# Optimization experiments

Hardware: AMD Instinct MI355X
Metric: run time of the kernel (lower is better)

## Reference

```python
import jax, jax.numpy as jnp
import numpy as np

N, E, B = 30000, 100000, 1024
FXD, FXT, D, H, NOUT = 78, 954, 128, 10, 2


def setup_inputs() -> dict:
    key = jax.random.key(0)
    ks = jax.random.split(key, 24)
    rn = lambda i, shape, s=0.05: jax.random.normal(ks[i], shape, dtype=jnp.float32) * s
    z = lambda shape: jnp.zeros(shape, dtype=jnp.float32)
    batch = ((jnp.arange(N) * B) // N).astype(jnp.int32)  # sorted, every graph id present
    return {
        "x1": rn(0, (N, FXD), 1.0),
        "edge_index1": jax.random.randint(ks[1], (2, E), 0, N, dtype=jnp.int32),
        "batch1": batch,
        "x2": rn(2, (N, FXD), 1.0),
        "edge_index2": jax.random.randint(ks[3], (2, E), 0, N, dtype=jnp.int32),
        "batch2": batch,
        "cell": jax.random.uniform(ks[4], (B, FXT), dtype=jnp.float32),
        "W1": rn(5, (FXD, H * D)), "a_src1": rn(6, (1, H, D)), "a_dst1": rn(7, (1, H, D)), "b1": z((H * D,)),
        # GATConv2: 1280 -> 128, 1 head
        "W2": rn(8, (H * D, D)), "a_src2": rn(9, (1, 1, D)), "a_dst2": rn(10, (1, 1, D)), "b2": z((D,)),
        "Wg": rn(11, (D, D)), "bg": z((D,)),
        "Wr1": rn(12, (FXT, 2048)), "br1": z((2048,)),
        "Wr2": rn(13, (2048, 512)), "br2": z((512,)),
        "Wr3": rn(14, (512, 2 * D)), "br3": z((2 * D,)),
        "Wf1": rn(15, (4 * D, 1024)), "bf1": z((1024,)),
        "Wf2": rn(16, (1024, 512)), "bf2": z((512,)),
        "Wf3": rn(17, (512, 128)), "bf3": z((128,)),
        "Wo": rn(18, (128, NOUT)), "bo": z((NOUT,)),
    }


def gat_conv(x, src, dst, W, a_src, a_dst, bias, heads, ch):
    """PyG GATConv (v1), self-loops already included in src/dst. Concat heads."""
    n = x.shape[0]
    h = (x @ W).reshape(n, heads, ch)                      # [N,H,C]
    alpha_s = jnp.sum(h * a_src, axis=-1)                  # [N,H]
    alpha_d = jnp.sum(h * a_dst, axis=-1)                  # [N,H]
    e = jax.nn.leaky_relu(alpha_s[src] + alpha_d[dst], 0.2)  # [E',H]
    emax = jax.ops.segment_max(e, dst, num_segments=n)     # segment softmax over dst
    ex = jnp.exp(e - emax[dst])
    denom = jax.ops.segment_sum(ex, dst, num_segments=n)
    alpha = ex / (denom[dst] + 1e-16)                      # [E',H]
    msg = h[src] * alpha[:, :, None]                       # [E',H,C]
    out = jax.ops.segment_sum(msg, dst, num_segments=n)    # [N,H,C]
    return out.reshape(n, heads * ch) + bias


def _l2norm(x):
    return x / jnp.maximum(jnp.linalg.norm(x, axis=1, keepdims=True), 1e-12)


def reference(x1, edge_index1, batch1, x2, edge_index2, batch2, cell,
              W1, a_src1, a_dst1, b1, W2, a_src2, a_dst2, b2, Wg, bg,
              Wr1, br1, Wr2, br2, Wr3, br3, Wf1, bf1, Wf2, bf2, Wf3, bf3, Wo, bo):
    def branch(x, ei, batch):
        n = x.shape[0]
        loops = jnp.arange(n, dtype=ei.dtype)              # add_self_loops=True
        src = jnp.concatenate([ei[0], loops])
        dst = jnp.concatenate([ei[1], loops])
        h = jax.nn.elu(gat_conv(x, src, dst, W1, a_src1, a_dst1, b1, H, D))
        h = jax.nn.elu(gat_conv(h, src, dst, W2, a_src2, a_dst2, b2, 1, D))
        g = jax.ops.segment_max(h, batch, num_segments=B)  # global_max_pool
        return jax.nn.relu(g @ Wg + bg)

    v1 = branch(x1, edge_index1, batch1)
    v2 = branch(x2, edge_index2, batch2)
    c = _l2norm(cell)
    c = jax.nn.relu(c @ Wr1 + br1)
    c = jax.nn.relu(c @ Wr2 + br2)
    c = jax.nn.relu(c @ Wr3 + br3)
    xc = _l2norm(jnp.concatenate([v1, v2, c], axis=1))
    xc = jax.nn.relu(xc @ Wf1 + bf1)
    xc = jax.nn.relu(xc @ Wf2 + bf2)
    xc = jax.nn.relu(xc @ Wf3 + bf3)
    return xc @ Wo + bo
```

## Files before the change

kernel.cpp:

```cpp
#include <hip/hip_runtime.h>
#include <math.h>

typedef unsigned short ushort_t;
typedef __attribute__((ext_vector_type(8))) short short8;
typedef __attribute__((ext_vector_type(8))) unsigned short ushort8v;
typedef __attribute__((ext_vector_type(4))) float float4v;
typedef __attribute__((ext_vector_type(4))) unsigned short ushort4v;

#define MPAD 30016
#define H1STR 136

__device__ __forceinline__ float lrelu02(float v){ return v > 0.f ? v : 0.2f*v; }
__device__ __forceinline__ float elu_fast(float v){ return v > 0.f ? v : (__expf(v) - 1.f); }

__device__ __forceinline__ ushort_t f2bf(float x){
  unsigned u = __float_as_uint(x);
  return (ushort_t)((u + 0x7fffu + ((u >> 16) & 1u)) >> 16);
}
__device__ __forceinline__ float bf2f(ushort_t h){ return __uint_as_float(((unsigned)h) << 16); }

__device__ __forceinline__ void gll16(const void* g, void* l){
  __builtin_amdgcn_global_load_lds((const __attribute__((address_space(1))) void*)g,
                                   (__attribute__((address_space(3))) void*)l, 16, 0, 0);
}

__global__ void fill_int_k(int* p, int v, int n){
  int i = blockIdx.x*blockDim.x + threadIdx.x;
  if (i < n) p[i] = v;
}

__global__ void hist2_k(const int* __restrict__ ei1, const int* __restrict__ ei2,
                        int E, int N, int* deg){
  int idx = blockIdx.x*blockDim.x + threadIdx.x;
  if (idx < 2*E){
    int br = idx / E, e = idx - br*E;
    const int* ei = br ? ei2 : ei1;
    atomicAdd(&deg[br*N + ei[E + e]], 1);
  }
}

__global__ __launch_bounds__(1024)
void scanA_k(const int* __restrict__ deg, int* __restrict__ rowptr, int* __restrict__ bsum, int n){
  int br = blockIdx.y;
  int t = threadIdx.x;
  int i = blockIdx.x*1024 + t;
  __shared__ int s[1024];
  int v = (i < n) ? deg[br*n + i] : 0;
  s[t] = v; __syncthreads();
  for (int off = 1; off < 1024; off <<= 1){
    int x = (t >= off) ? s[t - off] : 0;
    __syncthreads();
    s[t] += x;
    __syncthreads();
  }
  if (i < n) rowptr[br*(n+1) + i] = s[t] - v;
  if (t == 1023) bsum[br*gridDim.x + blockIdx.x] = s[1023];
}

__global__ void scanB_k(int* bsum, int nb){
  int br = threadIdx.x;
  if (br < 2){
    int run = 0;
    for (int i = 0; i < nb; ++i){ int v = bsum[br*nb + i]; bsum[br*nb + i] = run; run += v; }
  }
}

__global__ __launch_bounds__(1024)
void scanC_k(const int* __restrict__ bsum, int* __restrict__ rowptr, int n, int nb, int total){
  int br = blockIdx.y;
  int i = blockIdx.x*1024 + threadIdx.x;
  int add = bsum[br*nb + blockIdx.x];
  if (i < n) rowptr[br*(n+1) + i] += add;
  if (i == 0) rowptr[br*(n+1) + n] = total;
}

__global__ void init_cursor_k(const int* __restrict__ rowptr, int* cursor, int N){
  int idx = blockIdx.x*blockDim.x + threadIdx.x;
  if (idx < 2*N){ int br = idx / N, i = idx - br*N; cursor[idx] = rowptr[br*(N+1) + i]; }
}

__global__ void fill_csr2_k(const int* __restrict__ ei1, const int* __restrict__ ei2,
                            int E, int N, int* cursor, int* csr){
  int idx = blockIdx.x*blockDim.x + threadIdx.x;
  if (idx < 2*E){
    int br = idx / E, e = idx - br*E;
    const int* ei = br ? ei2 : ei1;
    int dst = ei[E + e];
    int pos = atomicAdd(&cursor[br*N + dst], 1);
    csr[br*(E+N) + pos] = ei[e];
  }
}

__global__ void self_loop2_k(int* cursor, int* csr, int E, int N){
  int idx = blockIdx.x*blockDim.x + threadIdx.x;
  if (idx < 2*N){
    int br = idx / N, i = idx - br*N;
    int pos = atomicAdd(&cursor[br*N + i], 1);
    csr[br*(E+N) + pos] = i;
  }
}

__global__ void mkattn_k(const float* __restrict__ W1, const float* __restrict__ a_src1,
                         const float* __restrict__ a_dst1,
                         const float* __restrict__ W2, const float* __restrict__ a_src2,
                         const float* __restrict__ a_dst2,
                         float* As, float* Ad, float* vs, float* vd){
  int idx = blockIdx.x*blockDim.x + threadIdx.x;
  if (idx < 780){
    int f = idx / 10, h = idx % 10;
    float ss = 0.f, sd = 0.f;
    for (int c = 0; c < 128; ++c){
      float w = W1[f*1280 + h*128 + c];
      ss += w * a_src1[h*128 + c];
      sd += w * a_dst1[h*128 + c];
    }
    As[idx] = ss; Ad[idx] = sd;
  } else if (idx < 2060){
    int k = idx - 780;
    float ss = 0.f, sd = 0.f;
    for (int c = 0; c < 128; ++c){
      float w = W2[k*128 + c];
      ss += w * a_src2[c]; sd += w * a_dst2[c];
    }
    vs[k] = ss; vd[k] = sd;
  }
}

__global__ __launch_bounds__(256)
void alpha1b_k(const float* __restrict__ x1, const float* __restrict__ x2,
               const float* __restrict__ As, const float* __restrict__ Ad,
               float* as1, float* ad1, int n){
  __shared__ float sAs[780], sAd[780];
  int t = threadIdx.x;
  for (int k = t; k < 780; k += 256){ sAs[k] = As[k]; sAd[k] = Ad[k]; }
  __syncthreads();
  int idx = blockIdx.x*256 + t;
  if (idx >= 2*n) return;
  int br = idx / n, i = idx - br*n;
  const float* xr = (br ? x2 : x1) + (size_t)i*78;
  float ss[10], sd[10];
  #pragma unroll
  for (int h = 0; h < 10; ++h){ ss[h] = 0.f; sd[h] = 0.f; }
  for (int f = 0; f < 78; ++f){
    float xv = xr[f];
    #pragma unroll
    for (int h = 0; h < 10; ++h){
      ss[h] += xv * sAs[f*10 + h];
      sd[h] += xv * sAd[f*10 + h];
    }
  }
  #pragma unroll
  for (int h = 0; h < 10; ++h){
    as1[(size_t)idx*10 + h] = ss[h];
    ad1[(size_t)idx*10 + h] = sd[h];
  }
}

__global__ __launch_bounds__(64)
void gat1_agg_k(const int* __restrict__ rowptr, const int* __restrict__ csr,
                const float* __restrict__ x, const float* __restrict__ as1,
                const float* __restrict__ ad1, ushort_t* __restrict__ yh, int n){
  int i = blockIdx.x;
  int t = threadIdx.x;
  __shared__ float adi[10], mh[10], rden[10], wE[10], xs[78];
  int beg = rowptr[i], end = rowptr[i+1];
  if (t < 10){
    float a = ad1[i*10 + t];
    adi[t] = a;
    float m = -1e30f;
    for (int e = beg; e < end; ++e){
      int s = csr[e];
      m = fmaxf(m, lrelu02(as1[s*10 + t] + a));
    }
    float den = 0.f;
    for (int e = beg; e < end; ++e){
      int s = csr[e];
      den += __expf(lrelu02(as1[s*10 + t] + a) - m);
    }
    mh[t] = m; rden[t] = 1.f/(den + 1e-16f);
  }
  __syncthreads();
  float acc[13];
  int hh[13], cc[13];
  #pragma unroll
  for (int k = 0; k < 13; ++k){
    acc[k] = 0.f;
    int j = t + 64*k;
    hh[k] = (j < 780) ? (j/78) : 0;
    cc[k] = (j < 780) ? (j%78) : 0;
  }
  for (int e = beg; e < end; ++e){
    int s = csr[e];
    if (t < 10) wE[t] = __expf(lrelu02(as1[s*10 + t] + adi[t]) - mh[t]) * rden[t];
    for (int c = t; c < 78; c += 64) xs[c] = x[(long long)s*78 + c];
    __syncthreads();
    #pragma unroll
    for (int k = 0; k < 13; ++k){
      int j = t + 64*k;
      if (j < 780) acc[k] += wE[hh[k]] * xs[cc[k]];
    }
    __syncthreads();
  }
  #pragma unroll
  for (int k = 0; k < 13; ++k){
    int j = t + 64*k;
    if (j < 780) yh[((size_t)hh[k]*MPAD + i)*96 + cc[k]] = f2bf(acc[k]);
  }
  for (int p = t; p < 180; p += 64){
    int h = p/18, c = 78 + p%18;
    yh[((size_t)h*MPAD + i)*96 + c] = 0;
  }
}

__global__ __launch_bounds__(256)
void branch_conv_k(const ushort_t* __restrict__ y,
                   const ushort_t* __restrict__ W1h, const ushort_t* __restrict__ W1l,
                   const ushort_t* __restrict__ W2h, const ushort_t* __restrict__ W2l,
                   const float* __restrict__ b1, const float* __restrict__ vs,
                   const float* __restrict__ vd,
                   float* __restrict__ h2, float* __restrict__ as2, float* __restrict__ ad2,
                   int M){
  __shared__ ushort_t stage[2][10240];
  __shared__ ushort_t h1t[64*H1STR];
  __shared__ float red[256];

  int tid = threadIdx.x, lane = tid & 63, wave = tid >> 6;
  int row0 = blockIdx.x*64;
  int wm = (wave & 1)*32, wn = (wave >> 1)*64;
  int lr = lane & 15, quad = lane >> 4;
  int sr = lane >> 2;
  int skc = (((lane & 3) ^ ((lane >> 3) & 3)) * 8);
  int qs  = (quad ^ ((lr >> 1) & 3)) * 8;

  float4v acc2[2][4];
  #pragma unroll
  for (int i = 0; i < 2; ++i)
    #pragma unroll
    for (int j = 0; j < 4; ++j)
      acc2[i][j] = (float4v){0.f, 0.f, 0.f, 0.f};
  float rps[8], rpd[8];
  #pragma unroll
  for (int z = 0; z < 8; ++z){ rps[z] = 0.f; rpd[z] = 0.f; }

  for (int h = 0; h < 10; ++h){
    const ushort_t* gA   = y   + ((size_t)h*MPAD + row0 + wave*16 + sr)*96 + skc;
    const ushort_t* gB0h = W1h + ((size_t)(h*128 + wave*32      + sr))*96 + skc;
    const ushort_t* gB1h = W1h + ((size_t)(h*128 + wave*32 + 16 + sr))*96 + skc;
    const ushort_t* gB0l = W1l + ((size_t)(h*128 + wave*32      + sr))*96 + skc;
    const ushort_t* gB1l = W1l + ((size_t)(h*128 + wave*32 + 16 + sr))*96 + skc;
    const ushort_t* gC0h = W2h + ((size_t)(wave*32      + sr))*1280 + h*128 + skc;
    const ushort_t* gC1h = W2h + ((size_t)(wave*32 + 16 + sr))*1280 + h*128 + skc;
    const ushort_t* gC0l = W2l + ((size_t)(wave*32      + sr))*1280 + h*128 + skc;
    const ushort_t* gC1l = W2l + ((size_t)(wave*32 + 16 + sr))*1280 + h*128 + skc;

    auto issue1 = [&](int p, int kt){
      ushort_t* st = &stage[p][0];
      gll16(gA   + kt, st + wave*512);
      gll16(gB0h + kt, st + 2048 + wave*1024);
      gll16(gB1h + kt, st + 2048 + wave*1024 + 512);
      gll16(gB0l + kt, st + 6144 + wave*1024);
      gll16(gB1l + kt, st + 6144 + wave*1024 + 512);
    };
    auto issue2 = [&](int p, int kt){
      ushort_t* st = &stage[p][0];
      gll16(gC0h + kt, st + 2048 + wave*1024);
      gll16(gC1h + kt, st + 2048 + wave*1024 + 512);
      gll16(gC0l + kt, st + 6144 + wave*1024);
      gll16(gC1l + kt, st + 6144 + wave*1024 + 512);
    };

    __syncthreads();
    issue1(0, 0);
    float4v acc1[2][4];
    #pragma unroll
    for (int i = 0; i < 2; ++i)
      #pragma unroll
      for (int j = 0; j < 4; ++j)
        acc1[i][j] = (float4v){0.f, 0.f, 0.f, 0.f};
    int p = 0;
    #pragma unroll
    for (int it = 0; it < 3; ++it){
      __syncthreads();
      if (it < 2) issue1(p ^ 1, (it + 1)*32);
      const ushort_t* sm = &stage[p][0];
      short8 af[2], bhf[4], blf[4];
      #pragma unroll
      for (int t2 = 0; t2 < 2; ++t2)
        af[t2] = *(const short8*)&sm[(wm + t2*16 + lr)*32 + qs];
      #pragma unroll
      for (int j = 0; j < 4; ++j){
        int nb = (wn + j*16 + lr)*32 + qs;
        bhf[j] = *(const short8*)&sm[2048 + nb];
        blf[j] = *(const short8*)&sm[6144 + nb];
      }
      #pragma unroll
      for (int i = 0; i < 2; ++i)
        #pragma unroll
        for (int j = 0; j < 4; ++j){
          acc1[i][j] = __builtin_amdgcn_mfma_f32_16x16x32_bf16(af[i], blf[j], acc1[i][j], 0, 0, 0);
          acc1[i][j] = __builtin_amdgcn_mfma_f32_16x16x32_bf16(af[i], bhf[j], acc1[i][j], 0, 0, 0);
        }
      p ^= 1;
    }

    #pragma unroll
    for (int j = 0; j < 4; ++j){
      int col = wn + j*16 + lr;
      float bv  = b1[h*128 + col];
      float vsv = vs[h*128 + col];
      float vdv = vd[h*128 + col];
      #pragma unroll
      for (int i = 0; i < 2; ++i){
        #pragma unroll
        for (int r = 0; r < 4; ++r){
          float v = elu_fast(acc1[i][j][r] + bv);
          h1t[(wm + i*16 + quad*4 + r)*H1STR + col] = f2bf(v);
          rps[i*4 + r] += v * vsv;
          rpd[i*4 + r] += v * vdv;
        }
      }
    }
    __syncthreads();

    issue2(0, 0);
    p = 0;
    #pragma unroll
    for (int it = 0; it < 4; ++it){
      __syncthreads();
      if (it < 3) issue2(p ^ 1, (it + 1)*32);
      const ushort_t* sm = &stage[p][0];
      int kt = it*32;
      short8 af[2], bhf[4], blf[4];
      #pragma unroll
      for (int t2 = 0; t2 < 2; ++t2)
        af[t2] = *(const short8*)&h1t[(wm + t2*16 + lr)*H1STR + kt + quad*8];
      #pragma unroll
      for (int j = 0; j < 4; ++j){
        int nb = (wn + j*16 + lr)*32 + qs;
        bhf[j] = *(const short8*)&sm[2048 + nb];
        blf[j] = *(const short8*)&sm[6144 + nb];
      }
      #pragma unroll
      for (int i = 0; i < 2; ++i)
        #pragma unroll
        for (int j = 0; j < 4; ++j){
          acc2[i][j] = __builtin_amdgcn_mfma_f32_16x16x32_bf16(af[i], blf[j], acc2[i][j], 0, 0, 0);
          acc2[i][j] = __builtin_amdgcn_mfma_f32_16x16x32_bf16(af[i], bhf[j], acc2[i][j], 0, 0, 0);
        }
      p ^= 1;
    }
  }

  #pragma unroll
  for (int j = 0; j < 4; ++j){
    int col = wn + j*16 + lr;
    #pragma unroll
    for (int i = 0; i < 2; ++i){
      #pragma unroll
      for (int r = 0; r < 4; ++r){
        int row = row0 + wm + i*16 + quad*4 + r;
        if (row < M) h2[(size_t)row*128 + col] = acc2[i][j][r];
      }
    }
  }
  __syncthreads();
  #pragma unroll
  for (int z = 0; z < 8; ++z){
    float a = rps[z], d = rpd[z];
    #pragma unroll
    for (int mk = 1; mk <= 8; mk <<= 1){
      a += __shfl_xor(a, mk);
      d += __shfl_xor(d, mk);
    }
    if (lr == 0){
      int i = z >> 2, r = z & 3;
      int row = wm + i*16 + quad*4 + r;
      red[row*2 + (wave >> 1)] = a;
      red[128 + row*2 + (wave >> 1)] = d;
    }
  }
  __syncthreads();
  if (tid < 64){
    int grow = row0 + tid;
    if (grow < M){
      as2[grow] = red[tid*2] + red[tid*2 + 1];
      ad2[grow] = red[128 + tid*2] + red[128 + tid*2 + 1];
    }
  }
}

__global__ __launch_bounds__(64)
void gat2_agg_k(const int* __restrict__ rowptr, const int* __restrict__ csr,
                const float* __restrict__ h2, const float* __restrict__ as2,
                const float* __restrict__ ad2, const float* __restrict__ b2,
                float* __restrict__ h2e, int n){
  int i = blockIdx.x, t = threadIdx.x;
  int beg = rowptr[i], end = rowptr[i+1];
  float adi = ad2[i];
  float m = -1e30f;
  for (int e = beg; e < end; ++e) m = fmaxf(m, lrelu02(as2[csr[e]] + adi));
  float den = 0.f;
  for (int e = beg; e < end; ++e) den += __expf(lrelu02(as2[csr[e]] + adi) - m);
  float rden = 1.f/(den + 1e-16f);
  float a0 = 0.f, a1 = 0.f;
  for (int e = beg; e < end; ++e){
    int s = csr[e];
    float w = __expf(lrelu02(as2[s] + adi) - m) * rden;
    a0 += w * h2[(long long)s*128 + t];
    a1 += w * h2[(long long)s*128 + 64 + t];
  }
  h2e[(long long)i*128 + t]      = elu_fast(a0 + b2[t]);
  h2e[(long long)i*128 + 64 + t] = elu_fast(a1 + b2[64 + t]);
}

__global__ __launch_bounds__(128)
void pool_split_k(const float* __restrict__ h2e, const int* __restrict__ batch, int n,
                  ushort_t* __restrict__ ph, ushort_t* __restrict__ pl){
  int g = blockIdx.x, t = threadIdx.x;
  int lo = 0, hi = n;
  while (lo < hi){ int mid = (lo + hi) >> 1; if (batch[mid] < g) lo = mid + 1; else hi = mid; }
  int a = lo, b = n;
  while (a < b){ int mid = (a + b) >> 1; if (batch[mid] < g + 1) a = mid + 1; else b = mid; }
  float m = -1e30f;
  for (int i = lo; i < a; ++i) m = fmaxf(m, h2e[(long long)i*128 + t]);
  ushort_t h = f2bf(m);
  ph[g*128 + t] = h; pl[g*128 + t] = f2bf(m - bf2f(h));
}

__global__ __launch_bounds__(256)
void l2norm_split_k(const float* __restrict__ in, int cols, int Kp,
                    ushort_t* __restrict__ oh, ushort_t* __restrict__ ol){
  int r = blockIdx.x, t = threadIdx.x;
  __shared__ float s[256];
  __shared__ float scaleS;
  const float* rp = in + (size_t)r*cols;
  float p = 0.f;
  for (int k = t; k < cols; k += 256){ float v = rp[k]; p += v*v; }
  s[t] = p; __syncthreads();
  for (int o = 128; o > 0; o >>= 1){
    if (t < o) s[t] += s[t+o];
    __syncthreads();
  }
  if (t == 0) scaleS = 1.f / fmaxf(sqrtf(s[0]), 1e-12f);
  __syncthreads();
  float sc = scaleS;
  for (int k = t; k < Kp; k += 256){
    float v = (k < cols) ? rp[k]*sc : 0.f;
    ushort_t h = f2bf(v);
    size_t o2 = (size_t)r*Kp + k;
    oh[o2] = h; ol[o2] = f2bf(v - bf2f(h));
  }
}

__global__ void concat_k(const float* __restrict__ v1, const float* __restrict__ v2,
                         const float* __restrict__ c3, float* __restrict__ xcat, int B){
  int idx = blockIdx.x*blockDim.x + threadIdx.x;
  if (idx < B*512){
    int r = idx >> 9, c = idx & 511;
    float v;
    if (c < 128) v = v1[r*128 + c];
    else if (c < 256) v = v2[r*128 + (c - 128)];
    else v = c3[r*256 + (c - 256)];
    xcat[idx] = v;
  }
}

__global__ void act_split_k(const float* __restrict__ in, ushort_t* __restrict__ oh,
                            ushort_t* __restrict__ ol, int n){
  int i = blockIdx.x*blockDim.x + threadIdx.x;
  if (i < n){
    float v = fmaxf(in[i], 0.f);
    ushort_t h = f2bf(v);
    oh[i] = h; ol[i] = f2bf(v - bf2f(h));
  }
}

__device__ __forceinline__ void split_one(const float* __restrict__ W, int ldw, int colStride,
                                          int N, int K, int Np, int Kp,
                                          ushort_t* __restrict__ dh, ushort_t* __restrict__ dl,
                                          int idx){
  int n  = idx % Np;
  int r  = idx / Np;
  int k4 = r % (Kp >> 2);
  int b  = r / (Kp >> 2);
  size_t o = ((size_t)b*Np + n)*Kp + (size_t)k4*4;
  ushort4v hv, lv;
  #pragma unroll
  for (int kk = 0; kk < 4; ++kk){
    int k = k4*4 + kk;
    float v = (n < N && k < K) ? W[(size_t)k*ldw + (size_t)b*colStride + n] : 0.f;
    ushort_t h = f2bf(v);
    hv[kk] = h; lv[kk] = f2bf(v - bf2f(h));
  }
  *(ushort4v*)&dh[o] = hv;
  *(ushort4v*)&dl[o] = lv;
}

struct SplitTable {
  const float *W1, *W2, *Wg, *Wr1, *Wr2, *Wr3, *Wf1, *Wf2, *Wf3, *Wo;
  ushort_t *W1h,*W1l,*W2h,*W2l,*Wgh,*Wgl,*Wr1h,*Wr1l,*Wr2h,*Wr2l;
  ushort_t *Wr3h,*Wr3l,*Wf1h,*Wf1l,*Wf2h,*Wf2l,*Wf3h,*Wf3l,*Woh,*Wol;
};

__global__ void split_all_k(SplitTable T){
  int idx = blockIdx.x*blockDim.x + threadIdx.x;
  if      (idx <   30720) split_one(T.W1, 1280, 128, 128,   78,  128,   96, T.W1h, T.W1l, idx);
  else if (idx <   71680) split_one(T.W2,  128,   0, 128, 1280,  128, 1280, T.W2h, T.W2l, idx -   30720);
  else if (idx <   75776) split_one(T.Wg,  128,   0, 128,  128,  128,  128, T.Wgh, T.Wgl, idx -   71680);
  else if (idx <  567296) split_one(T.Wr1,2048,   0,2048,  954, 2048,  960, T.Wr1h,T.Wr1l,idx -   75776);
  else if (idx <  829440) split_one(T.Wr2, 512,   0, 512, 2048,  512, 2048, T.Wr2h,T.Wr2l,idx -  567296);
  else if (idx <  862208) split_one(T.Wr3, 256,   0, 256,  512,  256,  512, T.Wr3h,T.Wr3l,idx -  829440);
  else if (idx <  993280) split_one(T.Wf1,1024,   0,1024,  512, 1024,  512, T.Wf1h,T.Wf1l,idx -  862208);
  else if (idx < 1124352) split_one(T.Wf2, 512,   0, 512, 1024,  512, 1024, T.Wf2h,T.Wf2l,idx -  993280);
  else if (idx < 1140736) split_one(T.Wf3, 128,   0, 128,  512,  128,  512, T.Wf3h,T.Wf3l,idx - 1124352);
  else if (idx < 1142784) split_one(T.Wo,    2,   0,   2,  128,   64,  128, T.Woh, T.Wol, idx - 1140736);
}

__global__ __launch_bounds__(256)
void gemm_split(const ushort_t* __restrict__ Ahp, const ushort_t* __restrict__ Alp, int lda, long long sA,
                const ushort_t* __restrict__ Bhp, const ushort_t* __restrict__ Blp, int ldb, long long sB,
                float* __restrict__ C, ushort_t* __restrict__ Ch, ushort_t* __restrict__ Cl,
                int ldc, long long sC,
                const float* __restrict__ bias, int sBias,
                int M, int Nc, int K, int act, int outMode, int kSplit, int aSplit){
  int zb = blockIdx.z;
  int b = zb / kSplit, kc = zb - b*kSplit;
  Ahp += (long long)b*sA;
  Bhp += (long long)b*sB; Blp += (long long)b*sB;
  long long cOff = (long long)b*sC;
  int Kc = K / kSplit;
  int kb = kc*Kc;
  int nIter = Kc / 32;

  __shared__ ushort_t smem[18048];

  int tid = threadIdx.x, lane = tid & 63, wave = tid >> 6;
  int row0 = blockIdx.y*64, col0 = blockIdx.x*64;
  int wm = (wave & 1)*32, wn = (wave >> 1)*32;
  int lr = lane & 15, quad = lane >> 4;
  int qs = (quad ^ ((lr >> 1) & 3)) * 8;

  int srow = wave*16 + (lane >> 2);
  int skc  = (((lane & 3) ^ ((lane >> 3) & 3)) * 8);
  const ushort_t* gAh = Ahp + (long long)(row0 + srow)*lda + skc + kb;
  const ushort_t* gAl = aSplit ? (Alp + (long long)b*sA + (long long)(row0 + srow)*lda + skc + kb) : gAh;
  const ushort_t* gBh = Bhp + (long long)(col0 + srow)*ldb + skc + kb;
  const ushort_t* gBl = Blp + (long long)(col0 + srow)*ldb + skc + kb;

  float4v acc[2][2];
  #pragma unroll
  for (int i = 0; i < 2; ++i)
    #pragma unroll
    for (int j = 0; j < 2; ++j)
      acc[i][j] = (float4v){0.f, 0.f, 0.f, 0.f};

  auto issue = [&](int p, int kt){
    ushort_t* base = &smem[p*8192 + wave*512];
    gll16(gAh + kt, base);
    if (aSplit) gll16(gAl + kt, base + 2048);
    gll16(gBh + kt, base + 4096);
    gll16(gBl + kt, base + 6144);
  };

  issue(0, 0);
  int p = 0;
  for (int it = 0; it < nIter; ++it){
    __syncthreads();
    if (it + 1 < nIter) issue(p ^ 1, (it + 1)*32);
    const ushort_t* sm = &smem[p*8192];
    short8 ah[2], al[2], bh[2], bl[2];
    #pragma unroll
    for (int t2 = 0; t2 < 2; ++t2){
      int ao = (wm + t2*16 + lr)*32 + qs;
      int bo = (wn + t2*16 + lr)*32 + qs;
      ah[t2] = *(const short8*)&sm[ao];
      if (aSplit) al[t2] = *(const short8*)&sm[2048 + ao];
      bh[t2] = *(const short8*)&sm[4096 + bo];
      bl[t2] = *(const short8*)&sm[6144 + bo];
    }
    #pragma unroll
    for (int i = 0; i < 2; ++i)
      #pragma unroll
      for (int j = 0; j < 2; ++j){
        if (aSplit)
          acc[i][j] = __builtin_amdgcn_mfma_f32_16x16x32_bf16(al[i], bh[j], acc[i][j], 0, 0, 0);
        acc[i][j] = __builtin_amdgcn_mfma_f32_16x16x32_bf16(ah[i], bl[j], acc[i][j], 0, 0, 0);
        acc[i][j] = __builtin_amdgcn_mfma_f32_16x16x32_bf16(ah[i], bh[j], acc[i][j], 0, 0, 0);
      }
    p ^= 1;
  }
  __syncthreads();

  if (outMode == 0 || outMode == 2){
    #pragma unroll
    for (int j = 0; j < 2; ++j){
      int col = col0 + wn + j*16 + lr;
      if (col >= Nc) continue;
      float bv = (bias && kc == 0) ? bias[(long long)b*sBias + col] : 0.f;
      #pragma unroll
      for (int i = 0; i < 2; ++i){
        #pragma unroll
        for (int r = 0; r < 4; ++r){
          int row = row0 + wm + i*16 + quad*4 + r;
          if (row >= M) continue;
          float v = acc[i][j][r] + bv;
          if (act == 1) v = fmaxf(v, 0.f);
          else if (act == 2) v = elu_fast(v);
          long long o = cOff + (long long)row*ldc + col;
          if (outMode == 0) C[o] = v;
          else atomicAdd(&C[o], v);
        }
      }
    }
  } else {
    float* ftile = (float*)smem;
    #pragma unroll
    for (int i = 0; i < 2; ++i)
      #pragma unroll
      for (int j = 0; j < 2; ++j)
        #pragma unroll
        for (int r = 0; r < 4; ++r)
          ftile[(wm + i*16 + quad*4 + r)*68 + wn + j*16 + lr] = acc[i][j][r];
    __syncthreads();
    int row = tid >> 2, ch = (tid & 3)*16;
    int grow = row0 + row;
    if (grow < M){
      if (col0 + 64 <= Nc){
        long long o = cOff + (long long)grow*ldc + col0 + ch;
        #pragma unroll
        for (int g = 0; g < 2; ++g){
          ushort8v hv, lv;
          #pragma unroll
          for (int c = 0; c < 8; ++c){
            int cc2 = ch + g*8 + c;
            float v = ftile[row*68 + cc2];
            if (bias) v += bias[(long long)b*sBias + col0 + cc2];
            if (act == 1) v = fmaxf(v, 0.f);
            else if (act == 2) v = elu_fast(v);
            hv[c] = f2bf(v);
            lv[c] = f2bf(v - bf2f(hv[c]));
          }
          *(ushort8v*)&Ch[o + g*8] = hv;
          *(ushort8v*)&Cl[o + g*8] = lv;
        }
      } else {
        for (int c = 0; c < 16; ++c){
          int col = col0 + ch + c;
          if (col >= Nc) break;
          float v = ftile[row*68 + ch + c];
          if (bias) v += bias[(long long)b*sBias + col];
          if (act == 1) v = fmaxf(v, 0.f);
          else if (act == 2) v = elu_fast(v);
          long long o = cOff + (long long)grow*ldc + col;
          ushort_t h = f2bf(v);
          Ch[o] = h;
          Cl[o] = f2bf(v - bf2f(h));
        }
      }
    }
  }
}

extern "C" void kernel_launch(void* const* d_in, const int* in_sizes, int n_in,
                              void* d_out, int out_size, void* d_ws, size_t ws_size,
                              hipStream_t stream){
  const float* x1     = (const float*)d_in[0];
  const int*   ei1    = (const int*)  d_in[1];
  const int*   batch1 = (const int*)  d_in[2];
  const float* x2     = (const float*)d_in[3];
  const int*   ei2    = (const int*)  d_in[4];
  const int*   batch2 = (const int*)  d_in[5];
  const float* cell   = (const float*)d_in[6];
  const float* W1     = (const float*)d_in[7];
  const float* a_src1 = (const float*)d_in[8];
  const float* a_dst1 = (const float*)d_in[9];
  const float* b1     = (const float*)d_in[10];
  const float* W2     = (const float*)d_in[11];
  const float* a_src2 = (const float*)d_in[12];
  const float* a_dst2 = (const float*)d_in[13];
  const float* b2     = (const float*)d_in[14];
  const float* Wg     = (const float*)d_in[15];
  const float* bg     = (const float*)d_in[16];
  const float* Wr1    = (const float*)d_in[17];
  const float* br1    = (const float*)d_in[18];
  const float* Wr2    = (const float*)d_in[19];
  const float* br2    = (const float*)d_in[20];
  const float* Wr3    = (const float*)d_in[21];
  const float* br3    = (const float*)d_in[22];
  const float* Wf1    = (const float*)d_in[23];
  const float* bf1    = (const float*)d_in[24];
  const float* Wf2    = (const float*)d_in[25];
  const float* bf2    = (const float*)d_in[26];
  const float* Wf3    = (const float*)d_in[27];
  const float* bf3    = (const float*)d_in[28];
  const float* Wo     = (const float*)d_in[29];
  const float* bo     = (const float*)d_in[30];
  float* out = (float*)d_out;
  (void)n_in; (void)out_size; (void)ws_size;

  const int N  = in_sizes[0] / 78;
  const int E  = in_sizes[1] / 2;
  const int Bg = in_sizes[6] / 954;

  char* wsb = (char*)d_ws;
  size_t off = 0;
  auto alloc = [&](size_t bytes)->char*{
    char* p = wsb + off; off += ((bytes + 255)/256)*256; return p;
  };

  char* Yb = alloc((size_t)10*MPAD*96*2);
  ushort_t* yh = (ushort_t*)Yb;
  size_t yoff = 0;
  auto yalloc = [&](size_t bytes)->char*{
    char* p = Yb + yoff; yoff += ((bytes + 255)/256)*256; return p;
  };
  ushort_t* cnh  = (ushort_t*)yalloc((size_t)Bg*960*2);
  ushort_t* cnl  = (ushort_t*)yalloc((size_t)Bg*960*2);
  ushort_t* c1h  = (ushort_t*)yalloc((size_t)Bg*2048*2);
  ushort_t* c1l  = (ushort_t*)yalloc((size_t)Bg*2048*2);
  float*    c2f  = (float*)   yalloc((size_t)Bg*512*4);
  ushort_t* c2h  = (ushort_t*)yalloc((size_t)Bg*512*2);
  ushort_t* c2l  = (ushort_t*)yalloc((size_t)Bg*512*2);
  float*    c3   = (float*)   yalloc((size_t)Bg*256*4);
  float*    xcat = (float*)   yalloc((size_t)Bg*512*4);
  ushort_t* xcnh = (ushort_t*)yalloc((size_t)Bg*512*2);
  ushort_t* xcnl = (ushort_t*)yalloc((size_t)Bg*512*2);
  ushort_t* t1h  = (ushort_t*)yalloc((size_t)Bg*1024*2);
  ushort_t* t1l  = (ushort_t*)yalloc((size_t)Bg*1024*2);
  float*    t2f  = (float*)   yalloc((size_t)Bg*512*4);
  ushort_t* t2h  = (ushort_t*)yalloc((size_t)Bg*512*2);
  ushort_t* t2l  = (ushort_t*)yalloc((size_t)Bg*512*2);
  float*    t3f  = (float*)   yalloc((size_t)Bg*128*4);
  ushort_t* t3h  = (ushort_t*)yalloc((size_t)Bg*128*2);
  ushort_t* t3l  = (ushort_t*)yalloc((size_t)Bg*128*2);

  float* h2  = (float*)alloc((size_t)MPAD*128*4);
  float* h2e = (float*)alloc((size_t)MPAD*128*4);

  ushort_t* W1th = (ushort_t*)alloc((size_t)10*128*96*2);
  ushort_t* W1tl = (ushort_t*)alloc((size_t)10*128*96*2);
  ushort_t* W2th = (ushort_t*)alloc((size_t)128*1280*2);
  ushort_t* W2tl = (ushort_t*)alloc((size_t)128*1280*2);
  ushort_t* Wgth = (ushort_t*)alloc((size_t)128*128*2);
  ushort_t* Wgtl = (ushort_t*)alloc((size_t)128*128*2);
  ushort_t* Wr1th= (ushort_t*)alloc((size_t)2048*960*2);
  ushort_t* Wr1tl= (ushort_t*)alloc((size_t)2048*960*2);
  ushort_t* Wr2th= (ushort_t*)alloc((size_t)512*2048*2);
  ushort_t* Wr2tl= (ushort_t*)alloc((size_t)512*2048*2);
  ushort_t* Wr3th= (ushort_t*)alloc((size_t)256*512*2);
  ushort_t* Wr3tl= (ushort_t*)alloc((size_t)256*512*2);
  ushort_t* Wf1th= (ushort_t*)alloc((size_t)1024*512*2);
  ushort_t* Wf1tl= (ushort_t*)alloc((size_t)1024*512*2);
  ushort_t* Wf2th= (ushort_t*)alloc((size_t)512*1024*2);
  ushort_t* Wf2tl= (ushort_t*)alloc((size_t)512*1024*2);
  ushort_t* Wf3th= (ushort_t*)alloc((size_t)128*512*2);
  ushort_t* Wf3tl= (ushort_t*)alloc((size_t)128*512*2);
  ushort_t* Woth = (ushort_t*)alloc((size_t)64*128*2);
  ushort_t* Wotl = (ushort_t*)alloc((size_t)64*128*2);

  float* as1b = (float*)alloc((size_t)2*N*10*4);
  float* ad1b = (float*)alloc((size_t)2*N*10*4);
  float* as2  = (float*)alloc((size_t)N*4);
  float* ad2  = (float*)alloc((size_t)N*4);
  float* AsB  = (float*)alloc(780*4);
  float* AdB  = (float*)alloc(780*4);
  float* vs   = (float*)alloc(1280*4);
  float* vd   = (float*)alloc(1280*4);
  int* deg2    = (int*)alloc((size_t)2*N*4);
  int* rowptr2 = (int*)alloc((size_t)2*(N+1)*4);
  int* cursor2 = (int*)alloc((size_t)2*N*4);
  int* csr2    = (int*)alloc((size_t)2*(E+N)*4);
  int* bsum    = (int*)alloc((size_t)2*64*4);
  ushort_t* pooledh = (ushort_t*)alloc((size_t)Bg*128*2);
  ushort_t* pooledl = (ushort_t*)alloc((size_t)Bg*128*2);
  float* v1   = (float*)alloc((size_t)Bg*128*4);
  float* v2   = (float*)alloc((size_t)Bg*128*4);

  auto gemm = [&](const ushort_t* Ah_, const ushort_t* Al_, int lda, long long sA_,
                  const ushort_t* Bh_, const ushort_t* Bl_, int ldb, long long sB_,
                  float* C_, ushort_t* Ch_, ushort_t* Cl_, int ldc, long long sC_,
                  const float* bias_, int sBias_, int M_, int N_, int K_, int batch_,
                  int act_, int mode_, int kSplit_, int aSplit_){
    dim3 grid((N_ + 63)/64, (M_ + 63)/64, batch_*kSplit_);
    gemm_split<<<grid, 256, 0, stream>>>(Ah_, Al_, lda, sA_, Bh_, Bl_, ldb, sB_,
                                         C_, Ch_, Cl_, ldc, sC_, bias_, sBias_,
                                         M_, N_, K_, act_, mode_, kSplit_, aSplit_);
  };

  SplitTable T;
  T.W1 = W1; T.W2 = W2; T.Wg = Wg; T.Wr1 = Wr1; T.Wr2 = Wr2; T.Wr3 = Wr3;
  T.Wf1 = Wf1; T.Wf2 = Wf2; T.Wf3 = Wf3; T.Wo = Wo;
  T.W1h = W1th; T.W1l = W1tl; T.W2h = W2th; T.W2l = W2tl; T.Wgh = Wgth; T.Wgl = Wgtl;
  T.Wr1h = Wr1th; T.Wr1l = Wr1tl; T.Wr2h = Wr2th; T.Wr2l = Wr2tl;
  T.Wr3h = Wr3th; T.Wr3l = Wr3tl; T.Wf1h = Wf1th; T.Wf1l = Wf1tl;
  T.Wf2h = Wf2th; T.Wf2l = Wf2tl; T.Wf3h = Wf3th; T.Wf3l = Wf3tl;
  T.Woh = Woth; T.Wol = Wotl;
  split_all_k<<<(1142784 + 255)/256, 256, 0, stream>>>(T);
  mkattn_k<<<(2060 + 255)/256, 256, 0, stream>>>(W1, a_src1, a_dst1, W2, a_src2, a_dst2,
                                                 AsB, AdB, vs, vd);
  alpha1b_k<<<((2*N) + 255)/256, 256, 0, stream>>>(x1, x2, AsB, AdB, as1b, ad1b, N);

  const int NB = (N + 1023)/1024;
  fill_int_k<<<((2*N) + 255)/256, 256, 0, stream>>>(deg2, 1, 2*N);
  hist2_k<<<((2*E) + 255)/256, 256, 0, stream>>>(ei1, ei2, E, N, deg2);
  scanA_k<<<dim3(NB, 2), 1024, 0, stream>>>(deg2, rowptr2, bsum, N);
  scanB_k<<<1, 64, 0, stream>>>(bsum, NB);
  scanC_k<<<dim3(NB, 2), 1024, 0, stream>>>(bsum, rowptr2, N, NB, E + N);
  init_cursor_k<<<((2*N) + 255)/256, 256, 0, stream>>>(rowptr2, cursor2, N);
  fill_csr2_k<<<((2*E) + 255)/256, 256, 0, stream>>>(ei1, ei2, E, N, cursor2, csr2);
  self_loop2_k<<<((2*N) + 255)/256, 256, 0, stream>>>(cursor2, csr2, E, N);

  for (int br = 0; br < 2; ++br){
    const float* x   = br ? x2 : x1;
    const int* batch = br ? batch2 : batch1;
    float* vout      = br ? v2 : v1;
    const int* rowptr = rowptr2 + (size_t)br*(N+1);
    const int* csr    = csr2 + (size_t)br*(E+N);
    const float* as1  = as1b + (size_t)br*N*10;
    const float* ad1  = ad1b + (size_t)br*N*10;

    gat1_agg_k<<<N, 64, 0, stream>>>(rowptr, csr, x, as1, ad1, yh, N);
    branch_conv_k<<<MPAD/64, 256, 0, stream>>>(yh, W1th, W1tl, W2th, W2tl,
                                               b1, vs, vd, h2, as2, ad2, N);
    gat2_agg_k<<<N, 64, 0, stream>>>(rowptr, csr, h2, as2, ad2, b2, h2e, N);
    pool_split_k<<<Bg, 128, 0, stream>>>(h2e, batch, N, pooledh, pooledl);
    gemm(pooledh, pooledl, 128, 0, Wgth, Wgtl, 128, 0,
         vout, nullptr, nullptr, 128, 0, bg, 0, Bg, 128, 128, 1, 1, 0, 1, 1);
  }

  l2norm_split_k<<<Bg, 256, 0, stream>>>(cell, 954, 960, cnh, cnl);
  gemm(cnh, cnl, 960, 0, Wr1th, Wr1tl, 960, 0, nullptr, c1h, c1l, 2048, 0,
       br1, 0, Bg, 2048, 960, 1, 1, 1, 1, 1);
  hipMemsetAsync(c2f, 0, (size_t)Bg*512*4, stream);
  gemm(c1h, c1l, 2048, 0, Wr2th, Wr2tl, 2048, 0, c2f, nullptr, nullptr, 512, 0,
       br2, 0, Bg, 512, 2048, 1, 0, 2, 4, 1);
  act_split_k<<<((Bg*512) + 255)/256, 256, 0, stream>>>(c2f, c2h, c2l, Bg*512);
  gemm(c2h, c2l, 512, 0, Wr3th, Wr3tl, 512, 0, c3, nullptr, nullptr, 256, 0,
       br3, 0, Bg, 256, 512, 1, 1, 0, 1, 1);

  concat_k<<<((Bg*512) + 255)/256, 256, 0, stream>>>(v1, v2, c3, xcat, Bg);
  l2norm_split_k<<<Bg, 256, 0, stream>>>(xcat, 512, 512, xcnh, xcnl);
  gemm(xcnh, xcnl, 512, 0, Wf1th, Wf1tl, 512, 0, nullptr, t1h, t1l, 1024, 0,
       bf1, 0, Bg, 1024, 512, 1, 1, 1, 1, 1);
  hipMemsetAsync(t2f, 0, (size_t)Bg*512*4, stream);
  gemm(t1h, t1l, 1024, 0, Wf2th, Wf2tl, 1024, 0, t2f, nullptr, nullptr, 512, 0,
       bf2, 0, Bg, 512, 1024, 1, 0, 2, 4, 1);
  act_split_k<<<((Bg*512) + 255)/256, 256, 0, stream>>>(t2f, t2h, t2l, Bg*512);
  hipMemsetAsync(t3f, 0, (size_t)Bg*128*4, stream);
  gemm(t2h, t2l, 512, 0, Wf3th, Wf3tl, 512, 0, t3f, nullptr, nullptr, 128, 0,
       bf3, 0, Bg, 128, 512, 1, 0, 2, 4, 1);
  act_split_k<<<((Bg*128) + 255)/256, 256, 0, stream>>>(t3f, t3h, t3l, Bg*128);
  gemm(t3h, t3l, 128, 0, Woth, Wotl, 128, 0, out, nullptr, nullptr, 2, 0,
       bo, 0, Bg, 2, 128, 1, 0, 0, 1, 1);
}
```

Baseline: 686.8 us.

## Batch both GAT branches, use single-pass softmax, and fuse max-pool via atomics

Both graph branches now run in single launches of gat1_agg, branch_conv and gat2_agg by indexing the branch from the block id, which doubles grid sizes and cuts launches. The segment softmax becomes single-pass: it drops the max subtraction, accumulates unnormalized weights and the denominator together, and normalizes at the end. This removes two extra passes over each node's edges. Global max pooling moves into gat2_agg as atomicMax on order-preserving encoded floats, which removes the h2e buffer and the pool kernel. Smaller changes fold cursor init into scanC, merge concat with the l2norm, and replace three memsets with one. The unshifted exp can overflow if attention logits are large.

New measurement: 601.0 us. 12.5% less time.

```diff
diff --git a/kernel.cpp b/kernel.cpp
--- a/kernel.cpp
+++ b/kernel.cpp
@@ -18,6 +18,14 @@
   return (ushort_t)((u + 0x7fffu + ((u >> 16) & 1u)) >> 16);
 }
 __device__ __forceinline__ float bf2f(ushort_t h){ return __uint_as_float(((unsigned)h) << 16); }
+
+__device__ __forceinline__ unsigned encf(float f){
+  unsigned u = __float_as_uint(f);
+  return (u & 0x80000000u) ? ~u : (u | 0x80000000u);
+}
+__device__ __forceinline__ float decf(unsigned u){
+  return __uint_as_float((u >> 31) ? (u & 0x7FFFFFFFu) : ~u);
+}
 
 __device__ __forceinline__ void gll16(const void* g, void* l){
   __builtin_amdgcn_global_load_lds((const __attribute__((address_space(1))) void*)g,
@@ -66,17 +74,17 @@
 }
 
 __global__ __launch_bounds__(1024)
-void scanC_k(const int* __restrict__ bsum, int* __restrict__ rowptr, int n, int nb, int total){
+void scanC_k(const int* __restrict__ bsum, int* __restrict__ rowptr, int* __restrict__ cursor,
+             int n, int nb, int total){
   int br = blockIdx.y;
   int i = blockIdx.x*1024 + threadIdx.x;
   int add = bsum[br*nb + blockIdx.x];
-  if (i < n) rowptr[br*(n+1) + i] += add;
+  if (i < n){
+    int nv = rowptr[br*(n+1) + i] + add;
+    rowptr[br*(n+1) + i] = nv;
+    cursor[br*n + i] = nv;
+  }
   if (i == 0) rowptr[br*(n+1) + n] = total;
-}
-
-__global__ void init_cursor_k(const int* __restrict__ rowptr, int* cursor, int N){
-  int idx = blockIdx.x*blockDim.x + threadIdx.x;
-  if (idx < 2*N){ int br = idx / N, i = idx - br*N; cursor[idx] = rowptr[br*(N+1) + i]; }
 }
 
 __global__ void fill_csr2_k(const int* __restrict__ ei1, const int* __restrict__ ei2,
@@ -157,29 +165,25 @@
 }
 
 __global__ __launch_bounds__(64)
-void gat1_agg_k(const int* __restrict__ rowptr, const int* __restrict__ csr,
-                const float* __restrict__ x, const float* __restrict__ as1,
-                const float* __restrict__ ad1, ushort_t* __restrict__ yh, int n){
-  int i = blockIdx.x;
+void gat1_agg_k(const int* __restrict__ rowptr2, const int* __restrict__ csr2,
+                const float* __restrict__ x1, const float* __restrict__ x2,
+                const float* __restrict__ as1b, const float* __restrict__ ad1b,
+                ushort_t* __restrict__ yh, int n, int E){
+  int gi = blockIdx.x;
+  int br = (gi >= n) ? 1 : 0;
+  int i = gi - br*n;
   int t = threadIdx.x;
-  __shared__ float adi[10], mh[10], rden[10], wE[10], xs[78];
+  const int* rowptr = rowptr2 + (size_t)br*(n+1);
+  const int* csr    = csr2 + (size_t)br*(E+n);
+  const float* x    = br ? x2 : x1;
+  const float* as1  = as1b + (size_t)br*n*10;
+  ushort_t* yb      = yh + (size_t)br*10*MPAD*96;
+
+  __shared__ float adi[10], rden[10], wE[10], xs[78];
   int beg = rowptr[i], end = rowptr[i+1];
-  if (t < 10){
-    float a = ad1[i*10 + t];
-    adi[t] = a;
-    float m = -1e30f;
-    for (int e = beg; e < end; ++e){
-      int s = csr[e];
-      m = fmaxf(m, lrelu02(as1[s*10 + t] + a));
-    }
-    float den = 0.f;
-    for (int e = beg; e < end; ++e){
-      int s = csr[e];
-      den += __expf(lrelu02(as1[s*10 + t] + a) - m);
-    }
-    mh[t] = m; rden[t] = 1.f/(den + 1e-16f);
-  }
+  if (t < 10) adi[t] = ad1b[(size_t)gi*10 + t];
   __syncthreads();
+  float den = 0.f;
   float acc[13];
   int hh[13], cc[13];
   #pragma unroll
@@ -191,8 +195,11 @@
   }
   for (int e = beg; e < end; ++e){
     int s = csr[e];
-    if (t < 10) wE[t] = __expf(lrelu02(as1[s*10 + t] + adi[t]) - mh[t]) * rden[t];
-    for (int c = t; c < 78; c += 64) xs[c] = x[(long long)s*78 + c];
+    if (t < 10){
+      float w = __expf(lrelu02(as1[(size_t)s*10 + t] + adi[t]));
+      wE[t] = w; den += w;
+    }
+    for (int c = t; c < 78; c += 64) xs[c] = x[(size_t)s*78 + c];
     __syncthreads();
     #pragma unroll
     for (int k = 0; k < 13; ++k){
@@ -201,31 +208,41 @@
     }
     __syncthreads();
   }
+  if (t < 10) rden[t] = 1.f/(den + 1e-16f);
+  __syncthreads();
   #pragma unroll
   for (int k = 0; k < 13; ++k){
     int j = t + 64*k;
-    if (j < 780) yh[((size_t)hh[k]*MPAD + i)*96 + cc[k]] = f2bf(acc[k]);
+    if (j < 780) yb[((size_t)hh[k]*MPAD + i)*96 + cc[k]] = f2bf(acc[k]*rden[hh[k]]);
   }
   for (int p = t; p < 180; p += 64){
     int h = p/18, c = 78 + p%18;
-    yh[((size_t)h*MPAD + i)*96 + c] = 0;
+    yb[((size_t)h*MPAD + i)*96 + c] = 0;
   }
 }
 
 __global__ __launch_bounds__(256)
-void branch_conv_k(const ushort_t* __restrict__ y,
+void branch_conv_k(const ushort_t* __restrict__ yall,
                    const ushort_t* __restrict__ W1h, const ushort_t* __restrict__ W1l,
                    const ushort_t* __restrict__ W2h, const ushort_t* __restrict__ W2l,
                    const float* __restrict__ b1, const float* __restrict__ vs,
                    const float* __restrict__ vd,
-                   float* __restrict__ h2, float* __restrict__ as2, float* __restrict__ ad2,
-                   int M){
+                   float* __restrict__ h2all, float* __restrict__ as2all,
+                   float* __restrict__ ad2all, int M){
+  const int NBLK = MPAD/64;
+  int br = blockIdx.x / NBLK;
+  int bi = blockIdx.x - br*NBLK;
+  const ushort_t* y = yall + (size_t)br*10*MPAD*96;
+  float* h2  = h2all + (size_t)br*MPAD*128;
+  float* as2 = as2all + (size_t)br*MPAD;
+  float* ad2 = ad2all + (size_t)br*MPAD;
+
   __shared__ ushort_t stage[2][10240];
   __shared__ ushort_t h1t[64*H1STR];
   __shared__ float red[256];
 
   int tid = threadIdx.x, lane = tid & 63, wave = tid >> 6;
-  int row0 = blockIdx.x*64;
+  int row0 = bi*64;
   int wm = (wave & 1)*32, wn = (wave >> 1)*64;
   int lr = lane & 15, quad = lane >> 4;
   int sr = lane >> 2;
@@ -390,41 +407,46 @@
 }
 
 __global__ __launch_bounds__(64)
-void gat2_agg_k(const int* __restrict__ rowptr, const int* __restrict__ csr,
-                const float* __restrict__ h2, const float* __restrict__ as2,
-                const float* __restrict__ ad2, const float* __restrict__ b2,
-                float* __restrict__ h2e, int n){
-  int i = blockIdx.x, t = threadIdx.x;
+void gat2_agg_k(const int* __restrict__ rowptr2, const int* __restrict__ csr2,
+                const float* __restrict__ h2all, const float* __restrict__ as2all,
+                const float* __restrict__ ad2all, const float* __restrict__ b2,
+                const int* __restrict__ batch1, const int* __restrict__ batch2,
+                unsigned* __restrict__ poolKey, int n, int E, int Bg){
+  int gi = blockIdx.x;
+  int br = (gi >= n) ? 1 : 0;
+  int i = gi - br*n;
+  int t = threadIdx.x;
+  const int* rowptr = rowptr2 + (size_t)br*(n+1);
+  const int* csr    = csr2 + (size_t)br*(E+n);
+  const float* h2   = h2all + (size_t)br*MPAD*128;
+  const float* as2  = as2all + (size_t)br*MPAD;
+  float adi = ad2all[(size_t)br*MPAD + i];
   int beg = rowptr[i], end = rowptr[i+1];
-  float adi = ad2[i];
-  float m = -1e30f;
-  for (int e = beg; e < end; ++e) m = fmaxf(m, lrelu02(as2[csr[e]] + adi));
-  float den = 0.f;
-  for (int e = beg; e < end; ++e) den += __expf(lrelu02(as2[csr[e]] + adi) - m);
-  float rden = 1.f/(den + 1e-16f);
-  float a0 = 0.f, a1 = 0.f;
+  float den = 0.f, a0 = 0.f, a1 = 0.f;
   for (int e = beg; e < end; ++e){
     int s = csr[e];
-    float w = __expf(lrelu02(as2[s] + adi) - m) * rden;
-    a0 += w * h2[(long long)s*128 + t];
-    a1 += w * h2[(long long)s*128 + 64 + t];
-  }
-  h2e[(long long)i*128 + t]      = elu_fast(a0 + b2[t]);
-  h2e[(long long)i*128 + 64 + t] = elu_fast(a1 + b2[64 + t]);
-}
-
-__global__ __launch_bounds__(128)
-void pool_split_k(const float* __restrict__ h2e, const int* __restrict__ batch, int n,
-                  ushort_t* __restrict__ ph, ushort_t* __restrict__ pl){
-  int g = blockIdx.x, t = threadIdx.x;
-  int lo = 0, hi = n;
-  while (lo < hi){ int mid = (lo + hi) >> 1; if (batch[mid] < g) lo = mid + 1; else hi = mid; }
-  int a = lo, b = n;
-  while (a < b){ int mid = (a + b) >> 1; if (batch[mid] < g + 1) a = mid + 1; else b = mid; }
-  float m = -1e30f;
-  for (int i = lo; i < a; ++i) m = fmaxf(m, h2e[(long long)i*128 + t]);
-  ushort_t h = f2bf(m);
-  ph[g*128 + t] = h; pl[g*128 + t] = f2bf(m - bf2f(h));
+    float w = __expf(lrelu02(as2[s] + adi));
+    den += w;
+    a0 += w * h2[(size_t)s*128 + t];
+    a1 += w * h2[(size_t)s*128 + 64 + t];
+  }
+  float r = 1.f/(den + 1e-16f);
+  float o0 = elu_fast(a0*r + b2[t]);
+  float o1 = elu_fast(a1*r + b2[64 + t]);
+  int g = (br ? batch2 : batch1)[i];
+  unsigned* pk = poolKey + ((size_t)br*Bg + g)*128;
+  atomicMax(&pk[t], encf(o0));
+  atomicMax(&pk[64 + t], encf(o1));
+}
+
+__global__ void pool_decode_k(const unsigned* __restrict__ key,
+                              ushort_t* __restrict__ ph, ushort_t* __restrict__ pl, int n){
+  int i = blockIdx.x*blockDim.x + threadIdx.x;
+  if (i < n){
+    float v = decf(key[i]);
+    ushort_t h = f2bf(v);
+    ph[i] = h; pl[i] = f2bf(v - bf2f(h));
+  }
 }
 
 __global__ __launch_bounds__(256)
@@ -452,17 +474,31 @@
   }
 }
 
-__global__ void concat_k(const float* __restrict__ v1, const float* __restrict__ v2,
-                         const float* __restrict__ c3, float* __restrict__ xcat, int B){
-  int idx = blockIdx.x*blockDim.x + threadIdx.x;
-  if (idx < B*512){
-    int r = idx >> 9, c = idx & 511;
-    float v;
-    if (c < 128) v = v1[r*128 + c];
-    else if (c < 256) v = v2[r*128 + (c - 128)];
-    else v = c3[r*256 + (c - 256)];
-    xcat[idx] = v;
-  }
+__global__ __launch_bounds__(256)
+void catnorm_k(const float* __restrict__ vall, const float* __restrict__ c3,
+               ushort_t* __restrict__ oh, ushort_t* __restrict__ ol, int Bg){
+  int r = blockIdx.x, t = threadIdx.x;
+  __shared__ float s[256];
+  __shared__ float scaleS;
+  auto val = [&](int c)->float{
+    if (c < 128) return vall[(size_t)r*128 + c];
+    if (c < 256) return vall[((size_t)Bg + r)*128 + (c - 128)];
+    return c3[(size_t)r*256 + (c - 256)];
+  };
+  float v0 = val(t), v1 = val(t + 256);
+  s[t] = v0*v0 + v1*v1; __syncthreads();
+  for (int o = 128; o > 0; o >>= 1){
+    if (t < o) s[t] += s[t+o];
+    __syncthreads();
+  }
+  if (t == 0) scaleS = 1.f / fmaxf(sqrtf(s[0]), 1e-12f);
+  __syncthreads();
+  float sc = scaleS;
+  float a = v0*sc, b = v1*sc;
+  ushort_t ha = f2bf(a), hb = f2bf(b);
+  size_t o2 = (size_t)r*512;
+  oh[o2 + t] = ha;       ol[o2 + t] = f2bf(a - bf2f(ha));
+  oh[o2 + 256 + t] = hb; ol[o2 + 256 + t] = f2bf(b - bf2f(hb));
 }
 
 __global__ void act_split_k(const float* __restrict__ in, ushort_t* __restrict__ oh,
@@ -708,7 +744,7 @@
     char* p = wsb + off; off += ((bytes + 255)/256)*256; return p;
   };
 
-  char* Yb = alloc((size_t)10*MPAD*96*2);
+  char* Yb = alloc((size_t)2*10*MPAD*96*2);
   ushort_t* yh = (ushort_t*)Yb;
   size_t yoff = 0;
   auto yalloc = [&](size_t bytes)->char*{
@@ -718,24 +754,31 @@
   ushort_t* cnl  = (ushort_t*)yalloc((size_t)Bg*960*2);
   ushort_t* c1h  = (ushort_t*)yalloc((size_t)Bg*2048*2);
   ushort_t* c1l  = (ushort_t*)yalloc((size_t)Bg*2048*2);
-  float*    c2f  = (float*)   yalloc((size_t)Bg*512*4);
   ushort_t* c2h  = (ushort_t*)yalloc((size_t)Bg*512*2);
   ushort_t* c2l  = (ushort_t*)yalloc((size_t)Bg*512*2);
   float*    c3   = (float*)   yalloc((size_t)Bg*256*4);
-  float*    xcat = (float*)   yalloc((size_t)Bg*512*4);
   ushort_t* xcnh = (ushort_t*)yalloc((size_t)Bg*512*2);
   ushort_t* xcnl = (ushort_t*)yalloc((size_t)Bg*512*2);
   ushort_t* t1h  = (ushort_t*)yalloc((size_t)Bg*1024*2);
   ushort_t* t1l  = (ushort_t*)yalloc((size_t)Bg*1024*2);
-  float*    t2f  = (float*)   yalloc((size_t)Bg*512*4);
   ushort_t* t2h  = (ushort_t*)yalloc((size_t)Bg*512*2);
   ushort_t* t2l  = (ushort_t*)yalloc((size_t)Bg*512*2);
-  float*    t3f  = (float*)   yalloc((size_t)Bg*128*4);
   ushort_t* t3h  = (ushort_t*)yalloc((size_t)Bg*128*2);
   ushort_t* t3l  = (ushort_t*)yalloc((size_t)Bg*128*2);
-
-  float* h2  = (float*)alloc((size_t)MPAD*128*4);
-  float* h2e = (float*)alloc((size_t)MPAD*128*4);
+  ushort_t* pooledh = (ushort_t*)yalloc((size_t)2*Bg*128*2);
+  ushort_t* pooledl = (ushort_t*)yalloc((size_t)2*Bg*128*2);
+  float*    vall    = (float*)   yalloc((size_t)2*Bg*128*4);
+
+  size_t zElems = (size_t)Bg*512 + (size_t)Bg*512 + (size_t)Bg*128 + (size_t)2*Bg*128;
+  float* zbase = (float*)alloc(zElems*4);
+  float* c2f = zbase;
+  float* t2f = c2f + (size_t)Bg*512;
+  float* t3f = t2f + (size_t)Bg*512;
+  unsigned* poolKey = (unsigned*)(t3f + (size_t)Bg*128);
+
+  float* h2  = (float*)alloc((size_t)2*MPAD*128*4);
+  float* as2 = (float*)alloc((size_t)2*MPAD*4);
+  float* ad2 = (float*)alloc((size_t)2*MPAD*4);
 
   ushort_t* W1th = (ushort_t*)alloc((size_t)10*128*96*2);
   ushort_t* W1tl = (ushort_t*)alloc((size_t)10*128*96*2);
@@ -760,8 +803,6 @@
 
   float* as1b = (float*)alloc((size_t)2*N*10*4);
   float* ad1b = (float*)alloc((size_t)2*N*10*4);
-  float* as2  = (float*)alloc((size_t)N*4);
-  float* ad2  = (float*)alloc((size_t)N*4);
   float* AsB  = (float*)alloc(780*4);
   float* AdB  = (float*)alloc(780*4);
   float* vs   = (float*)alloc(1280*4);
@@ -771,10 +812,6 @@
   int* cursor2 = (int*)alloc((size_t)2*N*4);
   int* csr2    = (int*)alloc((size_t)2*(E+N)*4);
   int* bsum    = (int*)alloc((size_t)2*64*4);
-  ushort_t* pooledh = (ushort_t*)alloc((size_t)Bg*128*2);
-  ushort_t* pooledl = (ushort_t*)alloc((size_t)Bg*128*2);
-  float* v1   = (float*)alloc((size_t)Bg*128*4);
-  float* v2   = (float*)alloc((size_t)Bg*128*4);
 
   auto gemm = [&](const ushort_t* Ah_, const ushort_t* Al_, int lda, long long sA_,
                   const ushort_t* Bh_, const ushort_t* Bl_, int ldb, long long sB_,
@@ -787,6 +824,7 @@
                                          M_, N_, K_, act_, mode_, kSplit_, aSplit_);
   };
 
+  hipMemsetAsync(zbase, 0, zElems*4, stream);
   SplitTable T;
   T.W1 = W1; T.W2 = W2; T.Wg = Wg; T.Wr1 = Wr1; T.Wr2 = Wr2; T.Wr3 = Wr3;
   T.Wf1 = Wf1; T.Wf2 = Wf2; T.Wf3 = Wf3; T.Wo = Wo;
@@ -805,48 +843,34 @@
   hist2_k<<<((2*E) + 255)/256, 256, 0, stream>>>(ei1, ei2, E, N, deg2);
   scanA_k<<<dim3(NB, 2), 1024, 0, stream>>>(deg2, rowptr2, bsum, N);
   scanB_k<<<1, 64, 0, stream>>>(bsum, NB);
-  scanC_k<<<dim3(NB, 2), 1024, 0, stream>>>(bsum, rowptr2, N, NB, E + N);
-  init_cursor_k<<<((2*N) + 255)/256, 256, 0, stream>>>(rowptr2, cursor2, N);
+  scanC_k<<<dim3(NB, 2), 1024, 0, stream>>>(bsum, rowptr2, cursor2, N, NB, E + N);
   fill_csr2_k<<<((2*E) + 255)/256, 256, 0, stream>>>(ei1, ei2, E, N, cursor2, csr2);
   self_loop2_k<<<((2*N) + 255)/256, 256, 0, stream>>>(cursor2, csr2, E, N);
 
-  for (int br = 0; br < 2; ++br){
-    const float* x   = br ? x2 : x1;
-    const int* batch = br ? batch2 : batch1;
-    float* vout      = br ? v2 : v1;
-    const int* rowptr = rowptr2 + (size_t)br*(N+1);
-    const int* csr    = csr2 + (size_t)br*(E+N);
-    const float* as1  = as1b + (size_t)br*N*10;
-    const float* ad1  = ad1b + (size_t)br*N*10;
-
-    gat1_agg_k<<<N, 64, 0, stream>>>(rowptr, csr, x, as1, ad1, yh, N);
-    branch_conv_k<<<MPAD/64, 256, 0, stream>>>(yh, W1th, W1tl, W2th, W2tl,
-                                               b1, vs, vd, h2, as2, ad2, N);
-    gat2_agg_k<<<N, 64, 0, stream>>>(rowptr, csr, h2, as2, ad2, b2, h2e, N);
-    pool_split_k<<<Bg, 128, 0, stream>>>(h2e, batch, N, pooledh, pooledl);
-    gemm(pooledh, pooledl, 128, 0, Wgth, Wgtl, 128, 0,
-         vout, nullptr, nullptr, 128, 0, bg, 0, Bg, 128, 128, 1, 1, 0, 1, 1);
-  }
+  gat1_agg_k<<<2*N, 64, 0, stream>>>(rowptr2, csr2, x1, x2, as1b, ad1b, yh, N, E);
+  branch_conv_k<<<2*(MPAD/64), 256, 0, stream>>>(yh, W1th, W1tl, W2th, W2tl,
+                                                 b1, vs, vd, h2, as2, ad2, N);
+  gat2_agg_k<<<2*N, 64, 0, stream>>>(rowptr2, csr2, h2, as2, ad2, b2,
+                                     batch1, batch2, poolKey, N, E, Bg);
+  pool_decode_k<<<((2*Bg*128) + 255)/256, 256, 0, stream>>>(poolKey, pooledh, pooledl, 2*Bg*128);
+  gemm(pooledh, pooledl, 128, 0, Wgth, Wgtl, 128, 0,
+       vall, nullptr, nullptr, 128, 0, bg, 0, 2*Bg, 128, 128, 1, 1, 0, 1, 1);
 
   l2norm_split_k<<<Bg, 256, 0, stream>>>(cell, 954, 960, cnh, cnl);
   gemm(cnh, cnl, 960, 0, Wr1th, Wr1tl, 960, 0, nullptr, c1h, c1l, 2048, 0,
        br1, 0, Bg, 2048, 960, 1, 1, 1, 1, 1);
-  hipMemsetAsync(c2f, 0, (size_t)Bg*512*4, stream);
   gemm(c1h, c1l, 2048, 0, Wr2th, Wr2tl, 2048, 0, c2f, nullptr, nullptr, 512, 0,
        br2, 0, Bg, 512, 2048, 1, 0, 2, 4, 1);
   act_split_k<<<((Bg*512) + 255)/256, 256, 0, stream>>>(c2f, c2h, c2l, Bg*512);
   gemm(c2h, c2l, 512, 0, Wr3th, Wr3tl, 512, 0, c3, nullptr, nullptr, 256, 0,
        br3, 0, Bg, 256, 512, 1, 1, 0, 1, 1);
 
-  concat_k<<<((Bg*512) + 255)/256, 256, 0, stream>>>(v1, v2, c3, xcat, Bg);
-  l2norm_split_k<<<Bg, 256, 0, stream>>>(xcat, 512, 512, xcnh, xcnl);
+  catnorm_k<<<Bg, 256, 0, stream>>>(vall, c3, xcnh, xcnl, Bg);
   gemm(xcnh, xcnl, 512, 0, Wf1th, Wf1tl, 512, 0, nullptr, t1h, t1l, 1024, 0,
        bf1, 0, Bg, 1024, 512, 1, 1, 1, 1, 1);
-  hipMemsetAsync(t2f, 0, (size_t)Bg*512*4, stream);
   gemm(t1h, t1l, 1024, 0, Wf2th, Wf2tl, 1024, 0, t2f, nullptr, nullptr, 512, 0,
        bf2, 0, Bg, 512, 1024, 1, 0, 2, 4, 1);
   act_split_k<<<((Bg*512) + 255)/256, 256, 0, stream>>>(t2f, t2h, t2l, Bg*512);
-  hipMemsetAsync(t3f, 0, (size_t)Bg*128*4, stream);
   gemm(t2h, t2l, 512, 0, Wf3th, Wf3tl, 512, 0, t3f, nullptr, nullptr, 128, 0,
        bf3, 0, Bg, 128, 512, 1, 0, 2, 4, 1);
   act_split_k<<<((Bg*128) + 255)/256, 256, 0, stream>>>(t3f, t3h, t3l, Bg*128);
```
